# Optimization experiments

Measured on AMD Instinct MI355X. Metric: run time of the kernel, lower is better.

The kernel has to match this reference:

```python
import jax, jax.numpy as jnp
import numpy as np

N_NODES = 50000
N_EDGES = 625000
N_GRAPHS = 256
CH = 128
N_LAYERS = 3
N_OUT = 10


def setup_inputs() -> dict:
    key = jax.random.key(0)
    ks = jax.random.split(key, 10)
    x = jax.random.normal(ks[0], (N_NODES, CH), dtype=jnp.float32)
    edge_src = jax.random.randint(ks[1], (N_EDGES,), 0, N_NODES, dtype=jnp.int32)
    edge_dst = jax.random.randint(ks[2], (N_EDGES,), 0, N_NODES, dtype=jnp.int32)
    graph_id = jnp.sort(jax.random.randint(ks[3], (N_NODES,), 0, N_GRAPHS, dtype=jnp.int32))
    scale = 0.05
    conv_W = jax.random.normal(ks[4], (N_LAYERS, 3, CH, CH), dtype=jnp.float32) * scale
    conv_b = jnp.zeros((N_LAYERS, 3, CH), dtype=jnp.float32)
    d1_W = jax.random.normal(ks[5], (CH, CH), dtype=jnp.float32) * scale
    d1_b = jnp.zeros((CH,), dtype=jnp.float32)
    d2_W = jax.random.normal(ks[6], (CH, N_OUT), dtype=jnp.float32) * scale
    d2_b = jnp.zeros((N_OUT,), dtype=jnp.float32)
    return dict(x=x, edge_src=edge_src, edge_dst=edge_dst, graph_id=graph_id,
                conv_W=conv_W, conv_b=conv_b, d1_W=d1_W, d1_b=d1_b,
                d2_W=d2_W, d2_b=d2_b)


def _gin_conv(h, edge_src, edge_dst, W, b):
    # aggregate: A @ h via gather + scatter-add (unit edge weights)
    agg = jax.ops.segment_sum(h[edge_src], edge_dst, num_segments=N_NODES)
    # epsilon = 0 -> (1 + eps) * h + agg = h + agg
    z = h + agg
    # MLP: Dense(relu) -> Dense(relu) -> Dense(linear)
    z = jax.nn.relu(z @ W[0] + b[0])
    z = jax.nn.relu(z @ W[1] + b[1])
    z = z @ W[2] + b[2]
    return z


def reference(x, edge_src, edge_dst, graph_id, conv_W, conv_b, d1_W, d1_b, d2_W, d2_b):
    h = x
    for l in range(N_LAYERS):
        h = _gin_conv(h, edge_src, edge_dst, conv_W[l], conv_b[l])
    # GlobalAvgPool over disjoint graphs: segment mean
    sums = jax.ops.segment_sum(h, graph_id, num_segments=N_GRAPHS)
    counts = jax.ops.segment_sum(jnp.ones((h.shape[0],), h.dtype), graph_id,
                                 num_segments=N_GRAPHS)
    pooled = sums / jnp.maximum(counts, 1.0)[:, None]
    h = jax.nn.relu(pooled @ d1_W + d1_b)
    # dropout is identity at inference
    return jax.nn.softmax(h @ d2_W + d2_b, axis=-1)
```

## Files before the change

kernel.cpp:

```cpp
#include <hip/hip_runtime.h>
#include <hip/hip_bf16.h>
#include <math.h>

#define NN 50000
#define NE 625000
#define NG 256
#define CH 128
#define NPAD 50048

typedef __attribute__((ext_vector_type(8))) short short8;
typedef __attribute__((ext_vector_type(4))) float floatx4;

__device__ __forceinline__ float bf2f_lo(unsigned u) {
    union { unsigned i; float f; } c; c.i = u << 16; return c.f;
}
__device__ __forceinline__ float bf2f_hi(unsigned u) {
    union { unsigned i; float f; } c; c.i = u & 0xffff0000u; return c.f;
}
__device__ __forceinline__ float bfu2f(unsigned short us) {
    union { unsigned i; float f; } c; c.i = ((unsigned)us) << 16; return c.f;
}
__device__ __forceinline__ unsigned short f2bfu(float f) {
    __hip_bfloat16 b = __float2bfloat16(f);
    union { __hip_bfloat16 b; unsigned short u; } c; c.b = b; return c.u;
}


__global__ __launch_bounds__(256) void k_hist(const int* __restrict__ dst, int* __restrict__ counts, int n) {
    int e = blockIdx.x * 256 + threadIdx.x;
    if (e < n) atomicAdd(&counts[dst[e]], 1);
}

__global__ __launch_bounds__(256) void k_scan1(const int* __restrict__ counts, int* __restrict__ partial, int n) {
    __shared__ int s[256];
    int t = threadIdx.x;
    int i = blockIdx.x * 256 + t;
    s[t] = (i < n) ? counts[i] : 0;
    __syncthreads();
    for (int d = 128; d > 0; d >>= 1) {
        if (t < d) s[t] += s[t + d];
        __syncthreads();
    }
    if (t == 0) partial[blockIdx.x] = s[0];
}

__global__ __launch_bounds__(256) void k_scan2(const int* __restrict__ partial, int* __restrict__ blockoff, int nb) {
    __shared__ int s[256];
    int t = threadIdx.x;
    int v = (t < nb) ? partial[t] : 0;
    s[t] = v;
    __syncthreads();
    for (int d = 1; d < 256; d <<= 1) {
        int x = (t >= d) ? s[t - d] : 0;
        __syncthreads();
        s[t] += x;
        __syncthreads();
    }
    if (t < nb) blockoff[t] = s[t] - v;
}

__global__ __launch_bounds__(256) void k_scan3(const int* __restrict__ counts, const int* __restrict__ blockoff,
                                               int* __restrict__ offsets, int n) {
    __shared__ int s[256];
    int t = threadIdx.x;
    int i = blockIdx.x * 256 + t;
    int v = (i < n) ? counts[i] : 0;
    s[t] = v;
    __syncthreads();
    for (int d = 1; d < 256; d <<= 1) {
        int x = (t >= d) ? s[t - d] : 0;
        __syncthreads();
        s[t] += x;
        __syncthreads();
    }
    if (i < n) offsets[i] = s[t] - v + blockoff[blockIdx.x];
}

__global__ __launch_bounds__(256) void k_fill(const int* __restrict__ src, const int* __restrict__ dst,
                                              const int* __restrict__ offsets, int* __restrict__ cursor,
                                              int* __restrict__ srclist, int n) {
    int e = blockIdx.x * 256 + threadIdx.x;
    if (e < n) {
        int d = dst[e];
        int pos = atomicAdd(&cursor[d], 1);
        srclist[offsets[d] + pos] = src[e];
    }
}


__global__ __launch_bounds__(256) void k_prep_x(const float* __restrict__ x, unsigned short* __restrict__ hb, int n4) {
    int i = blockIdx.x * 256 + threadIdx.x;
    if (i < n4) {
        float4 v = *(const float4*)&x[i * 4];
        ushort4 o;
        o.x = f2bfu(v.x); o.y = f2bfu(v.y); o.z = f2bfu(v.z); o.w = f2bfu(v.w);
        *(ushort4*)&hb[i * 4] = o;
    }
}

__global__ __launch_bounds__(256) void k_prep_w(const float* __restrict__ W, unsigned short* __restrict__ Wt, int total) {
    int i = blockIdx.x * 256 + threadIdx.x;
    if (i < total) {
        int mat = i >> 14;
        int rem = i & 16383;
        int k = rem >> 7;
        int n = rem & 127;
        Wt[mat * 16384 + n * 128 + k] = f2bfu(W[i]);
    }
}


__global__ __launch_bounds__(256) void k_gather(const unsigned short* __restrict__ h, const int* __restrict__ srclist,
                                                const int* __restrict__ offsets, const int* __restrict__ counts,
                                                unsigned short* __restrict__ outb) {
    int t = threadIdx.x;
    int node = blockIdx.x * 16 + (t >> 4);
    int sub = t & 15;
    int off = offsets[node];
    int deg = counts[node];

    float acc[8];
    {
        uint4 v = *(const uint4*)&h[(size_t)node * CH + sub * 8];
        acc[0] = bf2f_lo(v.x); acc[1] = bf2f_hi(v.x);
        acc[2] = bf2f_lo(v.y); acc[3] = bf2f_hi(v.y);
        acc[4] = bf2f_lo(v.z); acc[5] = bf2f_hi(v.z);
        acc[6] = bf2f_lo(v.w); acc[7] = bf2f_hi(v.w);
    }
#define ACC8(v) \
    acc[0] += bf2f_lo(v.x); acc[1] += bf2f_hi(v.x); \
    acc[2] += bf2f_lo(v.y); acc[3] += bf2f_hi(v.y); \
    acc[4] += bf2f_lo(v.z); acc[5] += bf2f_hi(v.z); \
    acc[6] += bf2f_lo(v.w); acc[7] += bf2f_hi(v.w);
    int i = 0;
    for (; i + 3 < deg; i += 4) {
        int s0 = srclist[off + i];
        int s1 = srclist[off + i + 1];
        int s2 = srclist[off + i + 2];
        int s3 = srclist[off + i + 3];
        uint4 v0 = *(const uint4*)&h[(size_t)s0 * CH + sub * 8];
        uint4 v1 = *(const uint4*)&h[(size_t)s1 * CH + sub * 8];
        uint4 v2 = *(const uint4*)&h[(size_t)s2 * CH + sub * 8];
        uint4 v3 = *(const uint4*)&h[(size_t)s3 * CH + sub * 8];
        ACC8(v0) ACC8(v1) ACC8(v2) ACC8(v3)
    }
    for (; i < deg; i++) {
        int s0 = srclist[off + i];
        uint4 v0 = *(const uint4*)&h[(size_t)s0 * CH + sub * 8];
        ACC8(v0)
    }
#undef ACC8
    ushort4 o0, o1;
    o0.x = f2bfu(acc[0]); o0.y = f2bfu(acc[1]); o0.z = f2bfu(acc[2]); o0.w = f2bfu(acc[3]);
    o1.x = f2bfu(acc[4]); o1.y = f2bfu(acc[5]); o1.z = f2bfu(acc[6]); o1.w = f2bfu(acc[7]);
    *(ushort4*)&outb[(size_t)node * CH + sub * 8] = o0;
    *(ushort4*)&outb[(size_t)node * CH + sub * 8 + 4] = o1;
}


__global__ __launch_bounds__(256, 2) void k_layer(const unsigned short* __restrict__ A,
                                                  const unsigned short* __restrict__ Wt3,
                                                  const float* __restrict__ bias3,
                                                  unsigned short* __restrict__ outb,
                                                  float* __restrict__ pooled,
                                                  const int* __restrict__ gid,
                                                  int nrows, int poolMode) {
    __shared__ unsigned short buf[2][128 * 128];

    int t = threadIdx.x;
    int wave = t >> 6;
    int lane = t & 63;
    int q = lane >> 4;
    int ml = lane & 15;
    int waveM = (wave >> 1) * 64;
    int waveN = (wave & 1) * 64;
    int rowBase = blockIdx.x * 128;

#pragma unroll
    for (int iter = 0; iter < 8; iter++) {
        int fid = t + iter * 256;
        int row = fid >> 4;
        int c = fid & 15;
        int r = rowBase + row;
        if (r >= nrows) r = nrows - 1;
        uint4 v = *(const uint4*)&A[(size_t)r * CH + c * 8];
        *(uint4*)&buf[0][row * 128 + ((c ^ (row & 15)) << 3)] = v;
    }
    __syncthreads();

    int rd = 0;
    for (int st = 0; st < 3; st++) {
        const unsigned short* Wm = Wt3 + st * 16384;
        const float* bs = bias3 + st * 128;

        floatx4 acc[4][4];
#pragma unroll
        for (int mt = 0; mt < 4; mt++)
#pragma unroll
            for (int nt = 0; nt < 4; nt++) acc[mt][nt] = (floatx4){0.f, 0.f, 0.f, 0.f};

#pragma unroll
        for (int s = 0; s < 4; s++) {
            short8 a[4], b[4];
#pragma unroll
            for (int mt = 0; mt < 4; mt++) {
                int m = waveM + mt * 16 + ml;
                a[mt] = *(const short8*)&Wm[m * 128 + s * 32 + q * 8];
            }
#pragma unroll
            for (int nt = 0; nt < 4; nt++) {
                int node = waveN + nt * 16 + ml;
                b[nt] = *(const short8*)&buf[rd][node * 128 + (((4 * s + q) ^ ml) << 3)];
            }
#pragma unroll
            for (int mt = 0; mt < 4; mt++)
#pragma unroll
                for (int nt = 0; nt < 4; nt++)
                    acc[mt][nt] = __builtin_amdgcn_mfma_f32_16x16x32_bf16(a[mt], b[nt], acc[mt][nt], 0, 0, 0);
        }

        int wr = rd ^ 1;
        int relu = (st < 2);
        int cw_base = (waveM >> 3);
#pragma unroll
        for (int mt = 0; mt < 4; mt++) {
            float4 bv = *(const float4*)&bs[waveM + mt * 16 + q * 4];
            float bva[4] = {bv.x, bv.y, bv.z, bv.w};
#pragma unroll
            for (int nt = 0; nt < 4; nt++) {
                int node = waveN + nt * 16 + ml;
                ushort4 o;
                float v0 = acc[mt][nt][0] + bva[0];
                float v1 = acc[mt][nt][1] + bva[1];
                float v2 = acc[mt][nt][2] + bva[2];
                float v3 = acc[mt][nt][3] + bva[3];
                if (relu) {
                    v0 = v0 > 0.f ? v0 : 0.f;
                    v1 = v1 > 0.f ? v1 : 0.f;
                    v2 = v2 > 0.f ? v2 : 0.f;
                    v3 = v3 > 0.f ? v3 : 0.f;
                }
                o.x = f2bfu(v0); o.y = f2bfu(v1); o.z = f2bfu(v2); o.w = f2bfu(v3);
                int cw = (cw_base + 2 * mt + (q >> 1)) ^ ml;
                *(ushort4*)&buf[wr][node * 128 + (cw << 3) + (q & 1) * 4] = o;
            }
        }
        __syncthreads();
        rd = wr;
    }

    if (!poolMode) {
#pragma unroll
        for (int iter = 0; iter < 8; iter++) {
            int fid = t + iter * 256;
            int row = fid >> 4;
            int c = fid & 15;
            int r = rowBase + row;
            if (r < nrows) {
                uint4 v = *(const uint4*)&buf[rd][row * 128 + ((c ^ (row & 15)) << 3)];
                *(uint4*)&outb[(size_t)r * CH + c * 8] = v;
            }
        }
    } else {
        int c = t & 127;
        int half = t >> 7;
        int n0 = half * 64;
        float runsum = 0.f;
        int curg = -1;
        for (int n = n0; n < n0 + 64; n++) {
            int r = rowBase + n;
            if (r >= nrows) break;
            int g = gid[r];
            unsigned short u = buf[rd][n * 128 + ((((c >> 3) ^ (n & 15))) << 3) + (c & 7)];
            float v = bfu2f(u);
            if (g != curg) {
                if (curg >= 0) atomicAdd(&pooled[(size_t)curg * CH + c], runsum);
                curg = g;
                runsum = 0.f;
            }
            runsum += v;
        }
        if (curg >= 0) atomicAdd(&pooled[(size_t)curg * CH + c], runsum);
    }
}


__device__ int lowerb(const int* a, int n, int key) {
    int lo = 0, hi = n;
    while (lo < hi) {
        int mid = (lo + hi) >> 1;
        if (a[mid] < key) lo = mid + 1;
        else hi = mid;
    }
    return lo;
}

__global__ __launch_bounds__(128) void k_head(const float* __restrict__ pooled, const int* __restrict__ gid,
                                              const float* __restrict__ W1, const float* __restrict__ b1,
                                              const float* __restrict__ W2, const float* __restrict__ b2,
                                              float* __restrict__ out) {
    __shared__ float p[CH];
    __shared__ float h1[CH];
    __shared__ float lg[10];
    __shared__ int bounds[2];
    int b = blockIdx.x;
    int c = threadIdx.x;
    if (c == 0) bounds[0] = lowerb(gid, NN, b);
    if (c == 1) bounds[1] = lowerb(gid, NN, b + 1);
    __syncthreads();
    float cnt = (float)(bounds[1] - bounds[0]);
    if (cnt < 1.f) cnt = 1.f;
    p[c] = pooled[b * CH + c] / cnt;
    __syncthreads();
    float acc = b1[c];
    for (int k = 0; k < CH; k++) acc += p[k] * W1[k * CH + c];
    h1[c] = acc > 0.f ? acc : 0.f;
    __syncthreads();
    if (c < 10) {
        float a = b2[c];
        for (int k = 0; k < CH; k++) a += h1[k] * W2[k * 10 + c];
        lg[c] = a;
    }
    __syncthreads();
    if (c == 0) {
        float m = lg[0];
        for (int o = 1; o < 10; o++) m = fmaxf(m, lg[o]);
        float e[10];
        float s = 0.f;
        for (int o = 0; o < 10; o++) {
            e[o] = expf(lg[o] - m);
            s += e[o];
        }
        for (int o = 0; o < 10; o++) out[b * 10 + o] = e[o] / s;
    }
}


extern "C" void kernel_launch(void* const* d_in, const int* in_sizes, int n_in,
                              void* d_out, int out_size, void* d_ws, size_t ws_size,
                              hipStream_t stream) {
    const float* x    = (const float*)d_in[0];
    const int* esrc   = (const int*)d_in[1];
    const int* edst   = (const int*)d_in[2];
    const int* gid    = (const int*)d_in[3];
    const float* convW = (const float*)d_in[4];
    const float* convb = (const float*)d_in[5];
    const float* d1W  = (const float*)d_in[6];
    const float* d1b  = (const float*)d_in[7];
    const float* d2W  = (const float*)d_in[8];
    const float* d2b  = (const float*)d_in[9];
    float* out = (float*)d_out;

    char* ws = (char*)d_ws;
    size_t off = 0;
    auto alloc = [&](size_t bytes) -> void* {
        void* p = ws + off;
        off += (bytes + 255) & ~(size_t)255;
        return p;
    };
    unsigned short* hb = (unsigned short*)alloc((size_t)NPAD * CH * 2);
    unsigned short* gb = (unsigned short*)alloc((size_t)NPAD * CH * 2);

    unsigned short* Wt = (unsigned short*)alloc((size_t)9 * 128 * 128 * 2);
    int* counts   = (int*)alloc((size_t)NN * 4);
    int* offs     = (int*)alloc((size_t)NN * 4);
    int* cursor   = (int*)alloc((size_t)NN * 4);
    int* srclist  = (int*)alloc((size_t)NE * 4);
    int* partial  = (int*)alloc(256 * 4);
    int* blockoff = (int*)alloc(256 * 4);
    float* pooled = (float*)alloc((size_t)NG * CH * 4);

    hipMemsetAsync(counts, 0, (size_t)NN * 4, stream);
    hipMemsetAsync(cursor, 0, (size_t)NN * 4, stream);
    hipMemsetAsync(pooled, 0, (size_t)NG * CH * 4, stream);

    k_hist<<<(NE + 255) / 256, 256, 0, stream>>>(edst, counts, NE);
    int nb = (NN + 255) / 256;
    k_scan1<<<nb, 256, 0, stream>>>(counts, partial, NN);
    k_scan2<<<1, 256, 0, stream>>>(partial, blockoff, nb);
    k_scan3<<<nb, 256, 0, stream>>>(counts, blockoff, offs, NN);
    k_fill<<<(NE + 255) / 256, 256, 0, stream>>>(esrc, edst, offs, cursor, srclist, NE);

    k_prep_x<<<(NN * CH / 4 + 255) / 256, 256, 0, stream>>>(x, hb, NN * CH / 4);
    k_prep_w<<<(9 * 128 * 128 + 255) / 256, 256, 0, stream>>>(convW, Wt, 9 * 128 * 128);

    int nblk = (NN + 127) / 128;
    for (int l = 0; l < 3; l++) {
        k_gather<<<NN / 16, 256, 0, stream>>>(hb, srclist, offs, counts, gb);
        k_layer<<<nblk, 256, 0, stream>>>(gb, Wt + (size_t)l * 3 * 16384, convb + l * 3 * CH,
                                          hb, pooled, gid, NN, (l == 2) ? 1 : 0);
    }
    k_head<<<NG, 128, 0, stream>>>(pooled, gid, d1W, d1b, d2W, d2b, out);
}
```

Measured before the change: 321.7 us.

## Fuse neighbor gather into layer MLP kernel, writing aggregates straight to LDS

The separate gather kernel is removed. Each layer kernel now aggregates neighbor features for its 128-row tile directly into the swizzled shared-memory buffer, then runs the three-stage MLP. This avoids writing and re-reading an intermediate aggregate buffer and drops three launches. Ping-pong buffers replace in-place output so a layer never reads rows that another block is overwriting. The cost is that the gather now runs at the MLP kernel's occupancy (2 blocks per CU, 32KB LDS), which may hide irregular memory latency less well.

Result: slower. 354.1 us (+10.1%).

```diff
diff --git a/kernel.cpp b/kernel.cpp
--- a/kernel.cpp
+++ b/kernel.cpp
@@ -110,55 +110,10 @@
 }
 
 
-__global__ __launch_bounds__(256) void k_gather(const unsigned short* __restrict__ h, const int* __restrict__ srclist,
-                                                const int* __restrict__ offsets, const int* __restrict__ counts,
-                                                unsigned short* __restrict__ outb) {
-    int t = threadIdx.x;
-    int node = blockIdx.x * 16 + (t >> 4);
-    int sub = t & 15;
-    int off = offsets[node];
-    int deg = counts[node];
-
-    float acc[8];
-    {
-        uint4 v = *(const uint4*)&h[(size_t)node * CH + sub * 8];
-        acc[0] = bf2f_lo(v.x); acc[1] = bf2f_hi(v.x);
-        acc[2] = bf2f_lo(v.y); acc[3] = bf2f_hi(v.y);
-        acc[4] = bf2f_lo(v.z); acc[5] = bf2f_hi(v.z);
-        acc[6] = bf2f_lo(v.w); acc[7] = bf2f_hi(v.w);
-    }
-#define ACC8(v) \
-    acc[0] += bf2f_lo(v.x); acc[1] += bf2f_hi(v.x); \
-    acc[2] += bf2f_lo(v.y); acc[3] += bf2f_hi(v.y); \
-    acc[4] += bf2f_lo(v.z); acc[5] += bf2f_hi(v.z); \
-    acc[6] += bf2f_lo(v.w); acc[7] += bf2f_hi(v.w);
-    int i = 0;
-    for (; i + 3 < deg; i += 4) {
-        int s0 = srclist[off + i];
-        int s1 = srclist[off + i + 1];
-        int s2 = srclist[off + i + 2];
-        int s3 = srclist[off + i + 3];
-        uint4 v0 = *(const uint4*)&h[(size_t)s0 * CH + sub * 8];
-        uint4 v1 = *(const uint4*)&h[(size_t)s1 * CH + sub * 8];
-        uint4 v2 = *(const uint4*)&h[(size_t)s2 * CH + sub * 8];
-        uint4 v3 = *(const uint4*)&h[(size_t)s3 * CH + sub * 8];
-        ACC8(v0) ACC8(v1) ACC8(v2) ACC8(v3)
-    }
-    for (; i < deg; i++) {
-        int s0 = srclist[off + i];
-        uint4 v0 = *(const uint4*)&h[(size_t)s0 * CH + sub * 8];
-        ACC8(v0)
-    }
-#undef ACC8
-    ushort4 o0, o1;
-    o0.x = f2bfu(acc[0]); o0.y = f2bfu(acc[1]); o0.z = f2bfu(acc[2]); o0.w = f2bfu(acc[3]);
-    o1.x = f2bfu(acc[4]); o1.y = f2bfu(acc[5]); o1.z = f2bfu(acc[6]); o1.w = f2bfu(acc[7]);
-    *(ushort4*)&outb[(size_t)node * CH + sub * 8] = o0;
-    *(ushort4*)&outb[(size_t)node * CH + sub * 8 + 4] = o1;
-}
-
-
-__global__ __launch_bounds__(256, 2) void k_layer(const unsigned short* __restrict__ A,
+__global__ __launch_bounds__(256, 2) void k_layer(const unsigned short* __restrict__ hin,
+                                                  const int* __restrict__ srclist,
+                                                  const int* __restrict__ offsets,
+                                                  const int* __restrict__ counts,
                                                   const unsigned short* __restrict__ Wt3,
                                                   const float* __restrict__ bias3,
                                                   unsigned short* __restrict__ outb,
@@ -176,15 +131,54 @@
     int waveN = (wave & 1) * 64;
     int rowBase = blockIdx.x * 128;
 
-#pragma unroll
-    for (int iter = 0; iter < 8; iter++) {
-        int fid = t + iter * 256;
-        int row = fid >> 4;
-        int c = fid & 15;
-        int r = rowBase + row;
-        if (r >= nrows) r = nrows - 1;
-        uint4 v = *(const uint4*)&A[(size_t)r * CH + c * 8];
-        *(uint4*)&buf[0][row * 128 + ((c ^ (row & 15)) << 3)] = v;
+    {
+        int sub = t & 15;
+#pragma unroll
+        for (int chunk = 0; chunk < 8; chunk++) {
+            int nl = chunk * 16 + (t >> 4);
+            int r = rowBase + nl;
+            if (r >= nrows) r = nrows - 1;
+            int off = offsets[r];
+            int deg = counts[r];
+
+            float acc[8];
+            {
+                uint4 v = *(const uint4*)&hin[(size_t)r * CH + sub * 8];
+                acc[0] = bf2f_lo(v.x); acc[1] = bf2f_hi(v.x);
+                acc[2] = bf2f_lo(v.y); acc[3] = bf2f_hi(v.y);
+                acc[4] = bf2f_lo(v.z); acc[5] = bf2f_hi(v.z);
+                acc[6] = bf2f_lo(v.w); acc[7] = bf2f_hi(v.w);
+            }
+#define ACC8(v) \
+            acc[0] += bf2f_lo(v.x); acc[1] += bf2f_hi(v.x); \
+            acc[2] += bf2f_lo(v.y); acc[3] += bf2f_hi(v.y); \
+            acc[4] += bf2f_lo(v.z); acc[5] += bf2f_hi(v.z); \
+            acc[6] += bf2f_lo(v.w); acc[7] += bf2f_hi(v.w);
+            int i = 0;
+            for (; i + 3 < deg; i += 4) {
+                int s0 = srclist[off + i];
+                int s1 = srclist[off + i + 1];
+                int s2 = srclist[off + i + 2];
+                int s3 = srclist[off + i + 3];
+                uint4 v0 = *(const uint4*)&hin[(size_t)s0 * CH + sub * 8];
+                uint4 v1 = *(const uint4*)&hin[(size_t)s1 * CH + sub * 8];
+                uint4 v2 = *(const uint4*)&hin[(size_t)s2 * CH + sub * 8];
+                uint4 v3 = *(const uint4*)&hin[(size_t)s3 * CH + sub * 8];
+                ACC8(v0) ACC8(v1) ACC8(v2) ACC8(v3)
+            }
+            for (; i < deg; i++) {
+                int s0 = srclist[off + i];
+                uint4 v0 = *(const uint4*)&hin[(size_t)s0 * CH + sub * 8];
+                ACC8(v0)
+            }
+#undef ACC8
+            ushort4 o0, o1;
+            o0.x = f2bfu(acc[0]); o0.y = f2bfu(acc[1]); o0.z = f2bfu(acc[2]); o0.w = f2bfu(acc[3]);
+            o1.x = f2bfu(acc[4]); o1.y = f2bfu(acc[5]); o1.z = f2bfu(acc[6]); o1.w = f2bfu(acc[7]);
+            int base = nl * 128 + ((sub ^ (nl & 15)) << 3);
+            *(ushort4*)&buf[0][base] = o0;
+            *(ushort4*)&buf[0][base + 4] = o1;
+        }
     }
     __syncthreads();
 
@@ -359,7 +353,7 @@
         return p;
     };
     unsigned short* hb = (unsigned short*)alloc((size_t)NPAD * CH * 2);
-    unsigned short* gb = (unsigned short*)alloc((size_t)NPAD * CH * 2);
+    unsigned short* tb = (unsigned short*)alloc((size_t)NPAD * CH * 2);
 
     unsigned short* Wt = (unsigned short*)alloc((size_t)9 * 128 * 128 * 2);
     int* counts   = (int*)alloc((size_t)NN * 4);
@@ -385,10 +379,11 @@
     k_prep_w<<<(9 * 128 * 128 + 255) / 256, 256, 0, stream>>>(convW, Wt, 9 * 128 * 128);
 
     int nblk = (NN + 127) / 128;
-    for (int l = 0; l < 3; l++) {
-        k_gather<<<NN / 16, 256, 0, stream>>>(hb, srclist, offs, counts, gb);
-        k_layer<<<nblk, 256, 0, stream>>>(gb, Wt + (size_t)l * 3 * 16384, convb + l * 3 * CH,
-                                          hb, pooled, gid, NN, (l == 2) ? 1 : 0);
-    }
+    k_layer<<<nblk, 256, 0, stream>>>(hb, srclist, offs, counts, Wt + (size_t)0 * 3 * 16384,
+                                      convb + 0 * 3 * CH, tb, pooled, gid, NN, 0);
+    k_layer<<<nblk, 256, 0, stream>>>(tb, srclist, offs, counts, Wt + (size_t)1 * 3 * 16384,
+                                      convb + 1 * 3 * CH, hb, pooled, gid, NN, 0);
+    k_layer<<<nblk, 256, 0, stream>>>(hb, srclist, offs, counts, Wt + (size_t)2 * 3 * 16384,
+                                      convb + 2 * 3 * CH, nullptr, pooled, gid, NN, 1);
     k_head<<<NG, 128, 0, stream>>>(pooled, gid, d1W, d1b, d2W, d2b, out);
 }
```

## Halve layer-MLP tile to 64 rows with single LDS buffer and unroll gather by 8

Applied to the files above, without the earlier changes.

The fused per-layer MLP kernel now processes 64 nodes per block instead of 128. It uses a single 16KB shared buffer with an extra barrier in place of double buffering, and raises launch bounds to 4 blocks per CU. This is meant to improve occupancy and spread the ~782 blocks across CUs, at the cost of reloading the weights from global/L2 twice as often. The gather kernel's neighbor loop is unrolled by 8 with a 2-way tail to keep more independent loads in flight.

New measurement: 351.1 us. 1.09x slower.

```diff
diff --git a/kernel.cpp b/kernel.cpp
--- a/kernel.cpp
+++ b/kernel.cpp
@@ -133,20 +133,24 @@
     acc[4] += bf2f_lo(v.z); acc[5] += bf2f_hi(v.z); \
     acc[6] += bf2f_lo(v.w); acc[7] += bf2f_hi(v.w);
     int i = 0;
-    for (; i + 3 < deg; i += 4) {
-        int s0 = srclist[off + i];
-        int s1 = srclist[off + i + 1];
-        int s2 = srclist[off + i + 2];
-        int s3 = srclist[off + i + 3];
-        uint4 v0 = *(const uint4*)&h[(size_t)s0 * CH + sub * 8];
-        uint4 v1 = *(const uint4*)&h[(size_t)s1 * CH + sub * 8];
-        uint4 v2 = *(const uint4*)&h[(size_t)s2 * CH + sub * 8];
-        uint4 v3 = *(const uint4*)&h[(size_t)s3 * CH + sub * 8];
-        ACC8(v0) ACC8(v1) ACC8(v2) ACC8(v3)
-    }
-    for (; i < deg; i++) {
-        int s0 = srclist[off + i];
-        uint4 v0 = *(const uint4*)&h[(size_t)s0 * CH + sub * 8];
+    for (; i + 7 < deg; i += 8) {
+        uint4 v0 = *(const uint4*)&h[(size_t)srclist[off + i + 0] * CH + sub * 8];
+        uint4 v1 = *(const uint4*)&h[(size_t)srclist[off + i + 1] * CH + sub * 8];
+        uint4 v2 = *(const uint4*)&h[(size_t)srclist[off + i + 2] * CH + sub * 8];
+        uint4 v3 = *(const uint4*)&h[(size_t)srclist[off + i + 3] * CH + sub * 8];
+        uint4 v4 = *(const uint4*)&h[(size_t)srclist[off + i + 4] * CH + sub * 8];
+        uint4 v5 = *(const uint4*)&h[(size_t)srclist[off + i + 5] * CH + sub * 8];
+        uint4 v6 = *(const uint4*)&h[(size_t)srclist[off + i + 6] * CH + sub * 8];
+        uint4 v7 = *(const uint4*)&h[(size_t)srclist[off + i + 7] * CH + sub * 8];
+        ACC8(v0) ACC8(v1) ACC8(v2) ACC8(v3) ACC8(v4) ACC8(v5) ACC8(v6) ACC8(v7)
+    }
+    for (; i + 1 < deg; i += 2) {
+        uint4 v0 = *(const uint4*)&h[(size_t)srclist[off + i + 0] * CH + sub * 8];
+        uint4 v1 = *(const uint4*)&h[(size_t)srclist[off + i + 1] * CH + sub * 8];
+        ACC8(v0) ACC8(v1)
+    }
+    if (i < deg) {
+        uint4 v0 = *(const uint4*)&h[(size_t)srclist[off + i] * CH + sub * 8];
         ACC8(v0)
     }
 #undef ACC8
@@ -158,14 +162,14 @@
 }
 
 
-__global__ __launch_bounds__(256, 2) void k_layer(const unsigned short* __restrict__ A,
+__global__ __launch_bounds__(256, 4) void k_layer(const unsigned short* __restrict__ A,
                                                   const unsigned short* __restrict__ Wt3,
                                                   const float* __restrict__ bias3,
                                                   unsigned short* __restrict__ outb,
                                                   float* __restrict__ pooled,
                                                   const int* __restrict__ gid,
                                                   int nrows, int poolMode) {
-    __shared__ unsigned short buf[2][128 * 128];
+    __shared__ unsigned short buf[64 * 128];
 
     int t = threadIdx.x;
     int wave = t >> 6;
@@ -173,53 +177,52 @@
     int q = lane >> 4;
     int ml = lane & 15;
     int waveM = (wave >> 1) * 64;
-    int waveN = (wave & 1) * 64;
-    int rowBase = blockIdx.x * 128;
-
-#pragma unroll
-    for (int iter = 0; iter < 8; iter++) {
+    int waveN = (wave & 1) * 32;
+    int rowBase = blockIdx.x * 64;
+
+#pragma unroll
+    for (int iter = 0; iter < 4; iter++) {
         int fid = t + iter * 256;
         int row = fid >> 4;
         int c = fid & 15;
         int r = rowBase + row;
         if (r >= nrows) r = nrows - 1;
         uint4 v = *(const uint4*)&A[(size_t)r * CH + c * 8];
-        *(uint4*)&buf[0][row * 128 + ((c ^ (row & 15)) << 3)] = v;
-    }
-    __syncthreads();
-
-    int rd = 0;
+        *(uint4*)&buf[row * 128 + ((c ^ (row & 15)) << 3)] = v;
+    }
+    __syncthreads();
+
     for (int st = 0; st < 3; st++) {
         const unsigned short* Wm = Wt3 + st * 16384;
         const float* bs = bias3 + st * 128;
 
-        floatx4 acc[4][4];
+        floatx4 acc[4][2];
 #pragma unroll
         for (int mt = 0; mt < 4; mt++)
 #pragma unroll
-            for (int nt = 0; nt < 4; nt++) acc[mt][nt] = (floatx4){0.f, 0.f, 0.f, 0.f};
+            for (int nt = 0; nt < 2; nt++) acc[mt][nt] = (floatx4){0.f, 0.f, 0.f, 0.f};
 
 #pragma unroll
         for (int s = 0; s < 4; s++) {
-            short8 a[4], b[4];
+            short8 a[4], b[2];
 #pragma unroll
             for (int mt = 0; mt < 4; mt++) {
                 int m = waveM + mt * 16 + ml;
                 a[mt] = *(const short8*)&Wm[m * 128 + s * 32 + q * 8];
             }
 #pragma unroll
-            for (int nt = 0; nt < 4; nt++) {
+            for (int nt = 0; nt < 2; nt++) {
                 int node = waveN + nt * 16 + ml;
-                b[nt] = *(const short8*)&buf[rd][node * 128 + (((4 * s + q) ^ ml) << 3)];
+                b[nt] = *(const short8*)&buf[node * 128 + (((4 * s + q) ^ ml) << 3)];
             }
 #pragma unroll
             for (int mt = 0; mt < 4; mt++)
 #pragma unroll
-                for (int nt = 0; nt < 4; nt++)
+                for (int nt = 0; nt < 2; nt++)
                     acc[mt][nt] = __builtin_amdgcn_mfma_f32_16x16x32_bf16(a[mt], b[nt], acc[mt][nt], 0, 0, 0);
         }
-
-        int wr = rd ^ 1;
+        __syncthreads();
+
         int relu = (st < 2);
         int cw_base = (waveM >> 3);
 #pragma unroll
@@ -227,7 +230,7 @@
             float4 bv = *(const float4*)&bs[waveM + mt * 16 + q * 4];
             float bva[4] = {bv.x, bv.y, bv.z, bv.w};
 #pragma unroll
-            for (int nt = 0; nt < 4; nt++) {
+            for (int nt = 0; nt < 2; nt++) {
                 int node = waveN + nt * 16 + ml;
                 ushort4 o;
                 float v0 = acc[mt][nt][0] + bva[0];
@@ -242,36 +245,35 @@
                 }
                 o.x = f2bfu(v0); o.y = f2bfu(v1); o.z = f2bfu(v2); o.w = f2bfu(v3);
                 int cw = (cw_base + 2 * mt + (q >> 1)) ^ ml;
-                *(ushort4*)&buf[wr][node * 128 + (cw << 3) + (q & 1) * 4] = o;
-            }
-        }
-        __syncthreads();
-        rd = wr;
+                *(ushort4*)&buf[node * 128 + (cw << 3) + (q & 1) * 4] = o;
+            }
+        }
+        __syncthreads();
     }
 
     if (!poolMode) {
 #pragma unroll
-        for (int iter = 0; iter < 8; iter++) {
+        for (int iter = 0; iter < 4; iter++) {
             int fid = t + iter * 256;
             int row = fid >> 4;
             int c = fid & 15;
             int r = rowBase + row;
             if (r < nrows) {
-                uint4 v = *(const uint4*)&buf[rd][row * 128 + ((c ^ (row & 15)) << 3)];
+                uint4 v = *(const uint4*)&buf[row * 128 + ((c ^ (row & 15)) << 3)];
                 *(uint4*)&outb[(size_t)r * CH + c * 8] = v;
             }
         }
     } else {
         int c = t & 127;
         int half = t >> 7;
-        int n0 = half * 64;
+        int n0 = half * 32;
         float runsum = 0.f;
         int curg = -1;
-        for (int n = n0; n < n0 + 64; n++) {
+        for (int n = n0; n < n0 + 32; n++) {
             int r = rowBase + n;
             if (r >= nrows) break;
             int g = gid[r];
-            unsigned short u = buf[rd][n * 128 + ((((c >> 3) ^ (n & 15))) << 3) + (c & 7)];
+            unsigned short u = buf[n * 128 + ((((c >> 3) ^ (n & 15))) << 3) + (c & 7)];
             float v = bfu2f(u);
             if (g != curg) {
                 if (curg >= 0) atomicAdd(&pooled[(size_t)curg * CH + c], runsum);
@@ -384,11 +386,11 @@
     k_prep_x<<<(NN * CH / 4 + 255) / 256, 256, 0, stream>>>(x, hb, NN * CH / 4);
     k_prep_w<<<(9 * 128 * 128 + 255) / 256, 256, 0, stream>>>(convW, Wt, 9 * 128 * 128);
 
-    int nblk = (NN + 127) / 128;
+    int nblkL = (NN + 63) / 64;
     for (int l = 0; l < 3; l++) {
         k_gather<<<NN / 16, 256, 0, stream>>>(hb, srclist, offs, counts, gb);
-        k_layer<<<nblk, 256, 0, stream>>>(gb, Wt + (size_t)l * 3 * 16384, convb + l * 3 * CH,
-                                          hb, pooled, gid, NN, (l == 2) ? 1 : 0);
+        k_layer<<<nblkL, 256, 0, stream>>>(gb, Wt + (size_t)l * 3 * 16384, convb + l * 3 * CH,
+                                           hb, pooled, gid, NN, (l == 2) ? 1 : 0);
     }
     k_head<<<NG, 128, 0, stream>>>(pooled, gid, d1W, d1b, d2W, d2b, out);
 }
```
